# Kernel optimization log

Hardware: AMD Instinct MI355X
Metric: run time of the kernel (lower is better)

Reference implementation:

```python
import jax, jax.numpy as jnp
import numpy as np


def setup_inputs() -> dict:
    key = jax.random.key(0)
    k1, k2, k3, k4, k5 = jax.random.split(key, 5)
    B, A, FI = 4096, 256, 16   # batch, atoms, iso functions per atom
    Bo, FA = 512, 8            # bonds, aniso functions per bond
    return {
        "c_iso": jax.random.normal(k1, (B, A, FI), dtype=jnp.float32),
        "c_aniso": jax.random.normal(k2, (B, Bo, FA), dtype=jnp.float32),
        "int_iso": jax.random.uniform(k3, (B, A, FI), dtype=jnp.float32),
        "int_aniso": jax.random.uniform(k4, (B, Bo, FA), dtype=jnp.float32),
        "charge": jax.random.normal(k5, (B, A), dtype=jnp.float32),
    }


def reference(c_iso, c_aniso, int_iso, int_aniso, charge):
    # Bordered KKT system from the Lagrangian L(x,u) = (x-c)^T(x-c) - u (q^T x - Q):
    #   q^T x     = Q
    # Exact closed-form solution (Sherman-Morrison on the rank-1 border):
    #   u = 2 (Q - q^T c) / (q^T q),   x = c + (u/2) q
    B = c_iso.shape[0]
    c = jnp.concatenate([c_iso.reshape(B, -1), c_aniso.reshape(B, -1)], axis=1)   # [B, n]
    q = jnp.concatenate([int_iso.reshape(B, -1), int_aniso.reshape(B, -1)], axis=1)  # [B, n]
    Q = jnp.sum(charge, axis=1)                                                   # [B]
    qTc = jnp.einsum("bn,bn->b", q, c)
    qTq = jnp.einsum("bn,bn->b", q, q)
    u = 2.0 * (Q - qTc) / qTq                                                     # Lagrange multiplier [B]
    x = c + 0.5 * u[:, None] * q                                                  # [B, n]
    n_iso = c_iso.shape[1] * c_iso.shape[2]
    sol_iso = x[:, :n_iso].reshape(c_iso.shape)
    sol_aniso = x[:, n_iso:].reshape(c_aniso.shape)
    return (sol_iso, sol_aniso)
```

## Files before the change

### kernel.cpp

```cpp
#include <hip/hip_runtime.h>


#define HALF_N 4096
#define BLOCK  256
#define WPB    4
#define RPW    2

typedef float f4 __attribute__((ext_vector_type(4)));

__global__ __launch_bounds__(BLOCK, 4) void qp_charge_norm_kernel(
    const float* __restrict__ c_iso,
    const float* __restrict__ c_aniso,
    const float* __restrict__ q_iso,
    const float* __restrict__ q_aniso,
    const float* __restrict__ charge,
    float* __restrict__ out,
    int B)
{
    const int wave  = threadIdx.x >> 6;
    const int lane  = threadIdx.x & 63;
    const int gwave = blockIdx.x * WPB + wave;

    for (int i = 0; i < RPW; ++i) {
        const int b = gwave * RPW + i;
        if (b >= B) return;

        const f4* ci = (const f4*)(c_iso   + (size_t)b * HALF_N);
        const f4* ca = (const f4*)(c_aniso + (size_t)b * HALF_N);
        const f4* qi = (const f4*)(q_iso   + (size_t)b * HALF_N);
        const f4* qa = (const f4*)(q_aniso + (size_t)b * HALF_N);

        f4 ch = ((const f4*)(charge + (size_t)b * 256))[lane];

        float qc0 = 0.f, qc1 = 0.f, qq0 = 0.f, qq1 = 0.f;
#pragma unroll 8
        for (int j = 0; j < 16; ++j) {
            f4 c = ci[j * 64 + lane];
            f4 q = qi[j * 64 + lane];
            qc0 += q[0]*c[0] + q[1]*c[1] + q[2]*c[2] + q[3]*c[3];
            qq0 += q[0]*q[0] + q[1]*q[1] + q[2]*q[2] + q[3]*q[3];
        }
#pragma unroll 8
        for (int j = 0; j < 16; ++j) {
            f4 c = ca[j * 64 + lane];
            f4 q = qa[j * 64 + lane];
            qc1 += q[0]*c[0] + q[1]*c[1] + q[2]*c[2] + q[3]*c[3];
            qq1 += q[0]*q[0] + q[1]*q[1] + q[2]*q[2] + q[3]*q[3];
        }
        float qc = qc0 + qc1;
        float qq = qq0 + qq1;
        float Q  = ch[0] + ch[1] + ch[2] + ch[3];

#pragma unroll
        for (int off = 32; off > 0; off >>= 1) {
            qc += __shfl_xor(qc, off, 64);
            qq += __shfl_xor(qq, off, 64);
            Q  += __shfl_xor(Q,  off, 64);
        }
        const float h = (Q - qc) / qq;

        f4* oi = (f4*)(out + (size_t)b * HALF_N);
        f4* oa = (f4*)(out + (size_t)B * HALF_N + (size_t)b * HALF_N);
#pragma unroll 8
        for (int j = 0; j < 16; ++j) {
            f4 c = ci[j * 64 + lane];
            f4 q = qi[j * 64 + lane];
            oi[j * 64 + lane] = c + h * q;
        }
#pragma unroll 8
        for (int j = 0; j < 16; ++j) {
            f4 c = ca[j * 64 + lane];
            f4 q = qa[j * 64 + lane];
            oa[j * 64 + lane] = c + h * q;
        }
    }
}

extern "C" void kernel_launch(void* const* d_in, const int* in_sizes, int n_in,
                              void* d_out, int out_size, void* d_ws, size_t ws_size,
                              hipStream_t stream) {
    const float* c_iso   = (const float*)d_in[0];
    const float* c_aniso = (const float*)d_in[1];
    const float* q_iso   = (const float*)d_in[2];
    const float* q_aniso = (const float*)d_in[3];
    const float* charge  = (const float*)d_in[4];
    float* out = (float*)d_out;

    const int B = in_sizes[0] / HALF_N;

    const int grid = (B + WPB * RPW - 1) / (WPB * RPW);
    qp_charge_norm_kernel<<<grid, BLOCK, 0, stream>>>(
        c_iso, c_aniso, q_iso, q_aniso, charge, out, B);
}
```

Measured before the change: 339.7 us.

## Use one 512-thread block per row and stage inputs to avoid re-reading global memory

Each row is now handled by a whole 512-thread block instead of one wave handling two rows. Every input element is loaded from global memory once and kept in registers, with q and c_aniso also copied to LDS. The per-wave partial sums are combined through shared memory with a single barrier before the output is written. This removes the second global read pass over c and q, which roughly halved the input traffic, at the cost of a block-wide barrier and about 48KB of LDS per block, which limits occupancy.

Measured after the change: 320.7 us. -5.6%, faster.

```diff
diff --git a/kernel.cpp b/kernel.cpp
--- a/kernel.cpp
+++ b/kernel.cpp
@@ -2,13 +2,15 @@
 
 
 #define HALF_N 4096
-#define BLOCK  256
-#define WPB    4
-#define RPW    2
+#define BLOCK  512
 
 typedef float f4 __attribute__((ext_vector_type(4)));
 
-__global__ __launch_bounds__(BLOCK, 4) void qp_charge_norm_kernel(
+__device__ __forceinline__ float dot4(f4 a, f4 b) {
+    return a[0]*b[0] + a[1]*b[1] + a[2]*b[2] + a[3]*b[3];
+}
+
+__global__ __launch_bounds__(BLOCK, 6) void qp_charge_norm_kernel(
     const float* __restrict__ c_iso,
     const float* __restrict__ c_aniso,
     const float* __restrict__ q_iso,
@@ -17,63 +19,70 @@
     float* __restrict__ out,
     int B)
 {
-    const int wave  = threadIdx.x >> 6;
-    const int lane  = threadIdx.x & 63;
-    const int gwave = blockIdx.x * WPB + wave;
+    const int b    = blockIdx.x;
+    const int t    = threadIdx.x;
+    const int wave = t >> 6;
+    const int lane = t & 63;
 
-    for (int i = 0; i < RPW; ++i) {
-        const int b = gwave * RPW + i;
-        if (b >= B) return;
+    __shared__ f4    q_s[2048];
+    __shared__ f4    ca_s[1024];
+    __shared__ float part[24];
 
-        const f4* ci = (const f4*)(c_iso   + (size_t)b * HALF_N);
-        const f4* ca = (const f4*)(c_aniso + (size_t)b * HALF_N);
-        const f4* qi = (const f4*)(q_iso   + (size_t)b * HALF_N);
-        const f4* qa = (const f4*)(q_aniso + (size_t)b * HALF_N);
+    const f4* ci = (const f4*)(c_iso   + (size_t)b * HALF_N);
+    const f4* ca = (const f4*)(c_aniso + (size_t)b * HALF_N);
+    const f4* qi = (const f4*)(q_iso   + (size_t)b * HALF_N);
+    const f4* qa = (const f4*)(q_aniso + (size_t)b * HALF_N);
 
+    f4 ci0 = ci[t];       f4 ci1 = ci[t + 512];
+    f4 qi0 = qi[t];       f4 qi1 = qi[t + 512];
+    f4 ca0 = ca[t];       f4 ca1 = ca[t + 512];
+    f4 qa0 = qa[t];       f4 qa1 = qa[t + 512];
+
+    float qc = dot4(qi0, ci0) + dot4(qi1, ci1) + dot4(qa0, ca0) + dot4(qa1, ca1);
+    float qq = dot4(qi0, qi0) + dot4(qi1, qi1) + dot4(qa0, qa0) + dot4(qa1, qa1);
+
+    float Q = 0.0f;
+    if (wave == 0) {
         f4 ch = ((const f4*)(charge + (size_t)b * 256))[lane];
+        Q = ch[0] + ch[1] + ch[2] + ch[3];
+    }
 
-        float qc0 = 0.f, qc1 = 0.f, qq0 = 0.f, qq1 = 0.f;
-#pragma unroll 8
-        for (int j = 0; j < 16; ++j) {
-            f4 c = ci[j * 64 + lane];
-            f4 q = qi[j * 64 + lane];
-            qc0 += q[0]*c[0] + q[1]*c[1] + q[2]*c[2] + q[3]*c[3];
-            qq0 += q[0]*q[0] + q[1]*q[1] + q[2]*q[2] + q[3]*q[3];
-        }
-#pragma unroll 8
-        for (int j = 0; j < 16; ++j) {
-            f4 c = ca[j * 64 + lane];
-            f4 q = qa[j * 64 + lane];
-            qc1 += q[0]*c[0] + q[1]*c[1] + q[2]*c[2] + q[3]*c[3];
-            qq1 += q[0]*q[0] + q[1]*q[1] + q[2]*q[2] + q[3]*q[3];
-        }
-        float qc = qc0 + qc1;
-        float qq = qq0 + qq1;
-        float Q  = ch[0] + ch[1] + ch[2] + ch[3];
+    q_s[t]          = qi0;
+    q_s[t + 512]    = qi1;
+    q_s[1024 + t]   = qa0;
+    q_s[1536 + t]   = qa1;
+    ca_s[t]         = ca0;
+    ca_s[t + 512]   = ca1;
 
 #pragma unroll
-        for (int off = 32; off > 0; off >>= 1) {
-            qc += __shfl_xor(qc, off, 64);
-            qq += __shfl_xor(qq, off, 64);
-            Q  += __shfl_xor(Q,  off, 64);
-        }
-        const float h = (Q - qc) / qq;
+    for (int off = 32; off > 0; off >>= 1) {
+        qc += __shfl_xor(qc, off, 64);
+        qq += __shfl_xor(qq, off, 64);
+        Q  += __shfl_xor(Q,  off, 64);
+    }
+    if (lane == 0) {
+        part[wave * 3 + 0] = qc;
+        part[wave * 3 + 1] = qq;
+        part[wave * 3 + 2] = Q;
+    }
+    __syncthreads();
 
-        f4* oi = (f4*)(out + (size_t)b * HALF_N);
-        f4* oa = (f4*)(out + (size_t)B * HALF_N + (size_t)b * HALF_N);
-#pragma unroll 8
-        for (int j = 0; j < 16; ++j) {
-            f4 c = ci[j * 64 + lane];
-            f4 q = qi[j * 64 + lane];
-            oi[j * 64 + lane] = c + h * q;
-        }
-#pragma unroll 8
-        for (int j = 0; j < 16; ++j) {
-            f4 c = ca[j * 64 + lane];
-            f4 q = qa[j * 64 + lane];
-            oa[j * 64 + lane] = c + h * q;
-        }
+    float tqc = 0.0f, tqq = 0.0f, tQ = 0.0f;
+#pragma unroll
+    for (int w = 0; w < 8; ++w) {
+        tqc += part[w * 3 + 0];
+        tqq += part[w * 3 + 1];
+        tQ  += part[w * 3 + 2];
     }
+    const float h = (tQ - tqc) / tqq;
+
+    f4* oi = (f4*)(out + (size_t)b * HALF_N);
+    f4* oa = (f4*)(out + (size_t)B * HALF_N + (size_t)b * HALF_N);
+
+    oi[t]       = ci0          + h * q_s[t];
+    oi[t + 512] = ci1          + h * q_s[t + 512];
+    oa[t]       = ca_s[t]      + h * q_s[1024 + t];
+    oa[t + 512] = ca_s[t + 512] + h * q_s[1536 + t];
 }
 
 extern "C" void kernel_launch(void* const* d_in, const int* in_sizes, int n_in,
@@ -88,7 +97,6 @@
 
     const int B = in_sizes[0] / HALF_N;
 
-    const int grid = (B + WPB * RPW - 1) / (WPB * RPW);
-    qp_charge_norm_kernel<<<grid, BLOCK, 0, stream>>>(
+    qp_charge_norm_kernel<<<B, BLOCK, 0, stream>>>(
         c_iso, c_aniso, q_iso, q_aniso, charge, out, B);
 }
```
